# Optimization experiments

Hardware: AMD Instinct MI355X
Metric: run time of the kernel (lower is better)

Reference implementation:

```python
import jax, jax.numpy as jnp
import numpy as np
import math

T, B, D = 2048, 4, 1024
H, HD = 16, 64  # num_heads, head_dim


def _rope_cos_sin(t_len, head_dim):
    inv_freq = 1.0 / (10000.0 ** (jnp.arange(0, head_dim, 2, dtype=jnp.float32) / head_dim))
    t = jnp.arange(t_len, dtype=jnp.float32)
    freqs = jnp.einsum('i,j->ij', t, inv_freq)          # (T, HD/2)
    emb = jnp.concatenate([freqs, freqs], axis=-1)       # (T, HD)
    # broadcast over (T, B, H, HD)
    return jnp.cos(emb)[:, None, None, :], jnp.sin(emb)[:, None, None, :]


def _rotate_half(x):
    x1, x2 = jnp.split(x, 2, axis=-1)
    return jnp.concatenate([-x2, x1], axis=-1)


def setup_inputs() -> dict:
    key = jax.random.key(0)
    ks = jax.random.split(key, 5)
    x = jax.random.normal(ks[0], (T, B, D), dtype=jnp.float32)
    # causal mask: True = masked (future positions), shape (T, T)
    attention_mask = jnp.triu(jnp.ones((T, T), dtype=bool), k=1)
    W_qkv = jax.random.normal(ks[1], (3 * D, D), dtype=jnp.float32) * (1.0 / math.sqrt(D))
    b_qkv = jax.random.normal(ks[2], (3 * D,), dtype=jnp.float32) * 0.02
    W_out = jax.random.normal(ks[3], (D, D), dtype=jnp.float32) * (1.0 / math.sqrt(D))
    b_out = jax.random.normal(ks[4], (D,), dtype=jnp.float32) * 0.02
    return {"x": x, "attention_mask": attention_mask, "W_qkv": W_qkv,
            "b_qkv": b_qkv, "W_out": W_out, "b_out": b_out}


def reference(x, attention_mask, W_qkv, b_qkv, W_out, b_out):
    t_len, b_sz, d = x.shape
    qkv = x @ W_qkv.T + b_qkv                              # (T, B, 3D)
    q, k, v = jnp.split(qkv, 3, axis=-1)
    q = q.reshape(t_len, b_sz, H, HD)
    k = k.reshape(t_len, b_sz, H, HD)
    v = v.reshape(t_len, b_sz, H, HD)

    cos, sin = _rope_cos_sin(t_len, HD)
    q = q * cos + _rotate_half(q) * sin
    k = k * cos + _rotate_half(k) * sin

    scale = math.sqrt(HD)
    # scores: (B, H, T, S)
    scores = jnp.einsum('tbhd,sbhd->bhts', q, k) / scale
    scores = jnp.where(attention_mask[None, None, :, :], -jnp.inf, scores)
    probs = jax.nn.softmax(scores.astype(jnp.float32), axis=-1).astype(v.dtype)
    context = jnp.einsum('bhts,sbhd->tbhd', probs, v)      # (T, B, H, HD)
    context = context.reshape(t_len, b_sz, d)
    return context @ W_out.T + b_out
```

## Files before the change

kernel.cpp:

```cpp
#include <hip/hip_runtime.h>
#include <math.h>

#define T_LEN 2048
#define B_SZ 4
#define D_MODEL 1024
#define NH 16
#define HD 64
#define BH_TOT (B_SZ*NH)

typedef __attribute__((ext_vector_type(8))) short bf16x8;
typedef __attribute__((ext_vector_type(4))) float f32x4;
typedef __attribute__((ext_vector_type(8))) unsigned short u16x8;

union U8 { unsigned int u[4]; bf16x8 v; };

static __device__ __forceinline__ unsigned short f2bf(float f) {
  unsigned int x = __float_as_uint(f);
  x += 0x7fffu + ((x >> 16) & 1u);
  return (unsigned short)(x >> 16);
}
static __device__ __forceinline__ float bf2f(unsigned short u) {
  return __uint_as_float(((unsigned int)u) << 16);
}

__global__ __launch_bounds__(256) void cvt_bf16_kernel(const float* __restrict__ src,
                                                       unsigned short* __restrict__ dst,
                                                       int n8) {
  const int i = blockIdx.x * 256 + threadIdx.x;
  if (i >= n8) return;
  const float4 a = ((const float4*)src)[i * 2];
  const float4 b = ((const float4*)src)[i * 2 + 1];
  u16x8 o;
  o[0] = f2bf(a.x); o[1] = f2bf(a.y); o[2] = f2bf(a.z); o[3] = f2bf(a.w);
  o[4] = f2bf(b.x); o[5] = f2bf(b.y); o[6] = f2bf(b.z); o[7] = f2bf(b.w);
  ((u16x8*)dst)[i] = o;
}

__global__ __launch_bounds__(256, 2) void gemm_mfma_kernel(
    const unsigned short* __restrict__ A, const unsigned short* __restrict__ W,
    const float* __restrict__ bias, float* __restrict__ C,
    int M, int N, int K, int mode,
    unsigned short* __restrict__ qd, unsigned short* __restrict__ kd,
    unsigned short* __restrict__ vd)
{
  __shared__ unsigned short As[128 * 64];
  __shared__ unsigned short Bs[128 * 64];
  const int tid = threadIdx.x;
  const int l = tid & 63, w = tid >> 6;
  const int lq = l & 15, lg = l >> 4;
  const int wm = w >> 1, wn = w & 1;
  const int n0 = blockIdx.x * 128, m0 = blockIdx.y * 128;

  const int sr = tid >> 3;
  const int sb = tid & 7;
  const int scol_src = sb << 4;
  const int scol_dst = scol_src ^ ((sr & 7) << 4);

  f32x4 acc[4][4];
#pragma unroll
  for (int mt = 0; mt < 4; ++mt)
#pragma unroll
    for (int nt = 0; nt < 4; ++nt)
#pragma unroll
      for (int r2 = 0; r2 < 4; ++r2) acc[mt][nt][r2] = 0.f;

  for (int k0 = 0; k0 < K; k0 += 64) {
    bf16x8 ar[4], br[4];
#pragma unroll
    for (int c = 0; c < 4; ++c) {
      const int row = c * 32 + sr;
      ar[c] = *(const bf16x8*)((const char*)A + ((size_t)(m0 + row) * K + k0) * 2 + scol_src);
      br[c] = *(const bf16x8*)((const char*)W + ((size_t)(n0 + row) * K + k0) * 2 + scol_src);
    }
    __syncthreads();
#pragma unroll
    for (int c = 0; c < 4; ++c) {
      const int row = c * 32 + sr;
      *(bf16x8*)((char*)As + row * 128 + scol_dst) = ar[c];
      *(bf16x8*)((char*)Bs + row * 128 + scol_dst) = br[c];
    }
    __syncthreads();

#pragma unroll
    for (int kc = 0; kc < 2; ++kc) {
      bf16x8 af[4], bfr[4];
#pragma unroll
      for (int mt = 0; mt < 4; ++mt) {
        const int r = wm * 64 + mt * 16 + lq;
        af[mt] = *(const bf16x8*)((const char*)As + r * 128 +
                                  ((kc * 64 + lg * 16) ^ ((r & 7) << 4)));
      }
#pragma unroll
      for (int nt = 0; nt < 4; ++nt) {
        const int r = wn * 64 + nt * 16 + lq;
        bfr[nt] = *(const bf16x8*)((const char*)Bs + r * 128 +
                                   ((kc * 64 + lg * 16) ^ ((r & 7) << 4)));
      }
#pragma unroll
      for (int mt = 0; mt < 4; ++mt)
#pragma unroll
        for (int nt = 0; nt < 4; ++nt)
          acc[mt][nt] = __builtin_amdgcn_mfma_f32_16x16x32_bf16(af[mt], bfr[nt], acc[mt][nt], 0, 0, 0);
    }
  }

  if (mode == 0) {
#pragma unroll
    for (int nt = 0; nt < 4; ++nt) {
      const int n = n0 + wn * 64 + nt * 16 + lq;
      const float bv = bias[n];
#pragma unroll
      for (int mt = 0; mt < 4; ++mt)
#pragma unroll
        for (int r2 = 0; r2 < 4; ++r2) {
          const int m = m0 + wm * 64 + mt * 16 + lg * 4 + r2;
          C[(size_t)m * N + n] = acc[mt][nt][r2] + bv;
        }
    }
  } else {
#pragma unroll
    for (int nt = 0; nt < 4; ++nt) {
      const int n = n0 + wn * 64 + nt * 16 + lq;
      const float bv = bias[n];
      const int which = n >> 10;
      const int h = (n >> 6) & (NH - 1);
      const int hd = n & 63;
      unsigned short* dst = (which == 0) ? qd : (which == 1) ? kd : vd;
#pragma unroll
      for (int mt = 0; mt < 4; ++mt)
#pragma unroll
        for (int r2 = 0; r2 < 4; ++r2) {
          const int m = m0 + wm * 64 + mt * 16 + lg * 4 + r2;
          const int t = m >> 2, b = m & 3;
          dst[((size_t)(b * NH + h) * T_LEN + t) * HD + hd] = f2bf(acc[mt][nt][r2] + bv);
        }
    }
  }
}

__global__ void rope_bf16_kernel(unsigned short* __restrict__ qb, unsigned short* __restrict__ kb)
{
  const int idx = blockIdx.x * blockDim.x + threadIdx.x;
  const int i  = idx & 31;
  const int t  = (idx >> 5) & (T_LEN - 1);
  const int bh = idx >> 16;
  const float inv_freq = powf(10000.f, -(float)i / 32.f);
  float s, c;
  sincosf((float)t * inv_freq, &s, &c);
  const size_t base = ((size_t)bh * T_LEN + t) * HD;
  const float q1 = bf2f(qb[base + i]), q2 = bf2f(qb[base + i + 32]);
  qb[base + i]      = f2bf((q1 * c - q2 * s) * 0.125f);
  qb[base + i + 32] = f2bf((q2 * c + q1 * s) * 0.125f);
  const float k1 = bf2f(kb[base + i]), k2 = bf2f(kb[base + i + 32]);
  kb[base + i]      = f2bf(k1 * c - k2 * s);
  kb[base + i + 32] = f2bf(k2 * c + k1 * s);
}

__global__ __launch_bounds__(256) void vtrans_kernel(const unsigned short* __restrict__ v,
                                                     unsigned short* __restrict__ vt)
{
  __shared__ unsigned short Ls[64][65];
  const int tid = threadIdx.x;
  const int bh = blockIdx.x, t0 = blockIdx.y * 64;
  {
    const int r = tid >> 2, c0 = (tid & 3) * 16;
    const unsigned short* src = v + ((size_t)bh * T_LEN + t0 + r) * HD + c0;
    u16x8 f0 = *(const u16x8*)src;
    u16x8 f1 = *(const u16x8*)(src + 8);
#pragma unroll
    for (int e = 0; e < 8; ++e) { Ls[r][c0 + e] = f0[e]; Ls[r][c0 + 8 + e] = f1[e]; }
  }
  __syncthreads();
  {
    const int d = tid >> 2, u0 = (tid & 3) * 16;
    u16x8 o0, o1;
#pragma unroll
    for (int e = 0; e < 8; ++e) { o0[e] = Ls[u0 + e][d]; o1[e] = Ls[u0 + 8 + e][d]; }
    unsigned short* dst = vt + ((size_t)bh * HD + d) * T_LEN + t0 + u0;
    *(u16x8*)dst = o0;
    *(u16x8*)(dst + 8) = o1;
  }
}

__global__ __launch_bounds__(256) void attn_mfma_kernel(
    const unsigned short* __restrict__ Qb,
    const unsigned short* __restrict__ Kb,
    const unsigned short* __restrict__ Vt,
    unsigned short* __restrict__ ctx)
{
  __shared__ unsigned short Ks[64 * 64];
  __shared__ unsigned short Vs[64 * 64];
  const int tid = threadIdx.x;
  const int l = tid & 63;
  const int w = tid >> 6;
  const int lq = l & 15, lg = l >> 4;
  const int bh = blockIdx.x, qbi = blockIdx.y;
  const int b = bh >> 4, h = bh & 15;
  const size_t tb = (size_t)bh * T_LEN;

  const int q0 = qbi * 64 + w * 16;
  bf16x8 qf0, qf1;
  {
    const unsigned short* qr = Qb + (tb + q0 + lq) * HD + lg * 8;
    qf0 = *(const bf16x8*)qr;
    qf1 = *(const bf16x8*)(qr + 32);
  }

  f32x4 acc[4];
#pragma unroll
  for (int dt = 0; dt < 4; ++dt)
#pragma unroll
    for (int r2 = 0; r2 < 4; ++r2) acc[dt][r2] = 0.f;
  float mrun = -1e30f, lsum = 0.f;
  const int qg = q0 + lq;

  for (int kbi = 0; kbi <= qbi; ++kbi) {
    const int s0 = kbi * 64;
    __syncthreads();
    {
      const int r = tid >> 3, c = tid & 7;
      const unsigned short* kg = Kb + (tb + s0 + r) * HD + c * 8;
      bf16x8 k0 = *(const bf16x8*)kg;
      bf16x8 k1 = *(const bf16x8*)(kg + 32 * HD);
      const unsigned short* vg = Vt + ((size_t)bh * HD + r) * T_LEN + s0 + c * 8;
      bf16x8 v0 = *(const bf16x8*)vg;
      bf16x8 v1 = *(const bf16x8*)(vg + 32 * T_LEN);
      const int xk = (c * 16) ^ ((r & 7) << 4);
      *(bf16x8*)((char*)Ks + r * 128 + xk)        = k0;
      *(bf16x8*)((char*)Ks + (r + 32) * 128 + xk) = k1;
      *(bf16x8*)((char*)Vs + r * 128 + xk)        = v0;
      *(bf16x8*)((char*)Vs + (r + 32) * 128 + xk) = v1;
    }
    __syncthreads();

    const bool diag = (kbi == qbi);
    const int stMax = diag ? (w + 1) : 4;

    f32x4 sv[4];
#pragma unroll
    for (int st = 0; st < 4; ++st)
#pragma unroll
      for (int r2 = 0; r2 < 4; ++r2) sv[st][r2] = -1e30f;

#pragma unroll
    for (int st = 0; st < 4; ++st) if (st < stMax) {
      const int r = st * 16 + lq;
      const int x = (r & 7) << 4;
      bf16x8 ka0 = *(const bf16x8*)((const char*)Ks + r * 128 + ((lg * 16) ^ x));
      bf16x8 ka1 = *(const bf16x8*)((const char*)Ks + r * 128 + (((lg + 4) * 16) ^ x));
      f32x4 z;
#pragma unroll
      for (int r2 = 0; r2 < 4; ++r2) z[r2] = 0.f;
      z = __builtin_amdgcn_mfma_f32_16x16x32_bf16(ka1, qf1, z, 0, 0, 0);
      z = __builtin_amdgcn_mfma_f32_16x16x32_bf16(ka0, qf0, z, 0, 0, 0);
      sv[st] = z;
    }

    if (diag) {
#pragma unroll
      for (int st = 0; st < 4; ++st)
#pragma unroll
        for (int r2 = 0; r2 < 4; ++r2) {
          const int sg = s0 + st * 16 + lg * 4 + r2;
          if (sg > qg) sv[st][r2] = -1e30f;
        }
    }

    float tmax = -1e30f;
#pragma unroll
    for (int st = 0; st < 4; ++st)
#pragma unroll
      for (int r2 = 0; r2 < 4; ++r2) tmax = fmaxf(tmax, sv[st][r2]);
    tmax = fmaxf(tmax, __shfl_xor(tmax, 16));
    tmax = fmaxf(tmax, __shfl_xor(tmax, 32));
    const float mnew = fmaxf(mrun, tmax);
    const float alpha = __expf(mrun - mnew);
    float p[4][4];
    float ps = 0.f;
#pragma unroll
    for (int st = 0; st < 4; ++st)
#pragma unroll
      for (int r2 = 0; r2 < 4; ++r2) {
        p[st][r2] = __expf(sv[st][r2] - mnew);
        ps += p[st][r2];
      }
    ps += __shfl_xor(ps, 16);
    ps += __shfl_xor(ps, 32);
    lsum = lsum * alpha + ps;
    mrun = mnew;

    float a4[4];
#pragma unroll
    for (int r2 = 0; r2 < 4; ++r2) a4[r2] = __shfl(alpha, lg * 4 + r2);
#pragma unroll
    for (int dt = 0; dt < 4; ++dt)
#pragma unroll
      for (int r2 = 0; r2 < 4; ++r2) acc[dt][r2] *= a4[r2];

    unsigned int lo[4], hi[4];
#pragma unroll
    for (int st = 0; st < 4; ++st) {
      asm("v_cvt_pk_bf16_f32 %0, %1, %2" : "=v"(lo[st]) : "v"(p[st][0]), "v"(p[st][1]));
      asm("v_cvt_pk_bf16_f32 %0, %1, %2" : "=v"(hi[st]) : "v"(p[st][2]), "v"(p[st][3]));
    }

    const int kcMax = diag ? ((w >> 1) + 1) : 2;
    const int srcA = lq + 32 * (lg & 1);
    const bool hiT = ((lg >> 1) & 1) != 0;
#pragma unroll
    for (int kc = 0; kc < 2; ++kc) if (kc < kcMax) {
      U8 pa;
      {
        unsigned int ta = __shfl(lo[2*kc], srcA),      tb2 = __shfl(lo[2*kc+1], srcA);
        pa.u[0] = hiT ? tb2 : ta;
      }
      {
        unsigned int ta = __shfl(hi[2*kc], srcA),      tb2 = __shfl(hi[2*kc+1], srcA);
        pa.u[1] = hiT ? tb2 : ta;
      }
      {
        unsigned int ta = __shfl(lo[2*kc], srcA + 16), tb2 = __shfl(lo[2*kc+1], srcA + 16);
        pa.u[2] = hiT ? tb2 : ta;
      }
      {
        unsigned int ta = __shfl(hi[2*kc], srcA + 16), tb2 = __shfl(hi[2*kc+1], srcA + 16);
        pa.u[3] = hiT ? tb2 : ta;
      }
#pragma unroll
      for (int dt = 0; dt < 4; ++dt) {
        const int d = dt * 16 + lq;
        bf16x8 vb = *(const bf16x8*)((const char*)Vs + d * 128 +
                                     (((4 * kc + lg) * 16) ^ ((d & 7) << 4)));
        acc[dt] = __builtin_amdgcn_mfma_f32_16x16x32_bf16(pa.v, vb, acc[dt], 0, 0, 0);
      }
    }
  }

  const float linv = 1.f / lsum;
  float l4[4];
#pragma unroll
  for (int r2 = 0; r2 < 4; ++r2) l4[r2] = __shfl(linv, lg * 4 + r2);
#pragma unroll
  for (int dt = 0; dt < 4; ++dt)
#pragma unroll
    for (int r2 = 0; r2 < 4; ++r2) {
      const int qrow = q0 + lg * 4 + r2;
      ctx[((size_t)qrow * B_SZ + b) * D_MODEL + h * HD + dt * 16 + lq] = f2bf(acc[dt][r2] * l4[r2]);
    }
}

extern "C" void kernel_launch(void* const* d_in, const int* in_sizes, int n_in,
                              void* d_out, int out_size, void* d_ws, size_t ws_size,
                              hipStream_t stream) {
  const float* x    = (const float*)d_in[0];
  const float* Wqkv = (const float*)d_in[2];
  const float* bqkv = (const float*)d_in[3];
  const float* Wout = (const float*)d_in[4];
  const float* bout = (const float*)d_in[5];
  float* out = (float*)d_out;

  char* wsb = (char*)d_ws;
  unsigned short* xb    = (unsigned short*)(wsb);
  unsigned short* wqkvb = (unsigned short*)(wsb + (22ull << 20)) - 3145728;
  unsigned short* woutb = (unsigned short*)(wsb + (22ull << 20));
  unsigned short* qb    = (unsigned short*)(wsb + (24ull << 20));
  unsigned short* kb    = (unsigned short*)(wsb + (40ull << 20));
  unsigned short* vb    = (unsigned short*)(wsb + (56ull << 20));
  unsigned short* vt    = (unsigned short*)(wsb + (72ull << 20));
  unsigned short* ctxb  = (unsigned short*)(wsb + (88ull << 20));

  cvt_bf16_kernel<<<(T_LEN*B_SZ*D_MODEL/8 + 255)/256, 256, 0, stream>>>(x, xb, T_LEN*B_SZ*D_MODEL/8);
  cvt_bf16_kernel<<<(3*D_MODEL*D_MODEL/8 + 255)/256, 256, 0, stream>>>(Wqkv, wqkvb, 3*D_MODEL*D_MODEL/8);
  cvt_bf16_kernel<<<(D_MODEL*D_MODEL/8 + 255)/256, 256, 0, stream>>>(Wout, woutb, D_MODEL*D_MODEL/8);

  dim3 g1(3 * D_MODEL / 128, (T_LEN * B_SZ) / 128);
  gemm_mfma_kernel<<<g1, 256, 0, stream>>>(xb, wqkvb, bqkv, nullptr,
                                           T_LEN * B_SZ, 3 * D_MODEL, D_MODEL, 1,
                                           qb, kb, vb);
  const int rope_total = BH_TOT * T_LEN * (HD / 2);
  rope_bf16_kernel<<<(rope_total + 255) / 256, 256, 0, stream>>>(qb, kb);

  dim3 gvt(BH_TOT, T_LEN / 64);
  vtrans_kernel<<<gvt, 256, 0, stream>>>(vb, vt);

  dim3 g2(BH_TOT, T_LEN / 64);
  attn_mfma_kernel<<<g2, 256, 0, stream>>>(qb, kb, vt, ctxb);

  dim3 g3(D_MODEL / 128, (T_LEN * B_SZ) / 128);
  gemm_mfma_kernel<<<g3, 256, 0, stream>>>(ctxb, woutb, bout, out,
                                           T_LEN * B_SZ, D_MODEL, D_MODEL, 0,
                                           nullptr, nullptr, nullptr);
}
```

Baseline: 223.3 us.

## Use direct global-to-LDS loads, double-buffer attention K/V, enlarge query tile

The GEMM staging now uses global_load_lds to write tiles straight into shared memory, skipping the round trip through registers. The attention kernel now gives each block 128 queries (two 16-row sub-tiles per wave) and double-buffers the K/V tiles, prefetching the next tile while computing the current one. Heavy causal blocks are scheduled first, and softmax uses exp2 with log2(e) folded into the Q scale. The rework raises register pressure and halves the attention grid, which may lower occupancy.

```diff
diff --git a/kernel.cpp b/kernel.cpp
--- a/kernel.cpp
+++ b/kernel.cpp
@@ -21,6 +21,10 @@
 }
 static __device__ __forceinline__ float bf2f(unsigned short u) {
   return __uint_as_float(((unsigned int)u) << 16);
+}
+static __device__ __forceinline__ void gload16(const void* g, void* l) {
+  __builtin_amdgcn_global_load_lds((const __attribute__((address_space(1))) void*)g,
+                                   (__attribute__((address_space(3))) void*)l, 16, 0, 0);
 }
 
 __global__ __launch_bounds__(256) void cvt_bf16_kernel(const float* __restrict__ src,
@@ -51,10 +55,8 @@
   const int wm = w >> 1, wn = w & 1;
   const int n0 = blockIdx.x * 128, m0 = blockIdx.y * 128;
 
-  const int sr = tid >> 3;
-  const int sb = tid & 7;
-  const int scol_src = sb << 4;
-  const int scol_dst = scol_src ^ ((sr & 7) << 4);
+  const int lrow = l >> 3;
+  const int lcolb = ((l & 7) << 4) ^ (lrow << 4);
 
   f32x4 acc[4][4];
 #pragma unroll
@@ -65,19 +67,15 @@
       for (int r2 = 0; r2 < 4; ++r2) acc[mt][nt][r2] = 0.f;
 
   for (int k0 = 0; k0 < K; k0 += 64) {
-    bf16x8 ar[4], br[4];
+    __syncthreads();
 #pragma unroll
     for (int c = 0; c < 4; ++c) {
-      const int row = c * 32 + sr;
-      ar[c] = *(const bf16x8*)((const char*)A + ((size_t)(m0 + row) * K + k0) * 2 + scol_src);
-      br[c] = *(const bf16x8*)((const char*)W + ((size_t)(n0 + row) * K + k0) * 2 + scol_src);
-    }
-    __syncthreads();
-#pragma unroll
-    for (int c = 0; c < 4; ++c) {
-      const int row = c * 32 + sr;
-      *(bf16x8*)((char*)As + row * 128 + scol_dst) = ar[c];
-      *(bf16x8*)((char*)Bs + row * 128 + scol_dst) = br[c];
+      const int r0 = w * 32 + c * 8;
+      const int row = r0 + lrow;
+      gload16((const char*)A + ((size_t)(m0 + row) * K + k0) * 2 + lcolb,
+              (char*)As + r0 * 128);
+      gload16((const char*)W + ((size_t)(n0 + row) * K + k0) * 2 + lcolb,
+              (char*)Bs + r0 * 128);
     }
     __syncthreads();
 
@@ -148,9 +146,10 @@
   float s, c;
   sincosf((float)t * inv_freq, &s, &c);
   const size_t base = ((size_t)bh * T_LEN + t) * HD;
+  const float QS = 0.18033688011112042f;
   const float q1 = bf2f(qb[base + i]), q2 = bf2f(qb[base + i + 32]);
-  qb[base + i]      = f2bf((q1 * c - q2 * s) * 0.125f);
-  qb[base + i + 32] = f2bf((q2 * c + q1 * s) * 0.125f);
+  qb[base + i]      = f2bf((q1 * c - q2 * s) * QS);
+  qb[base + i + 32] = f2bf((q2 * c + q1 * s) * QS);
   const float k1 = bf2f(kb[base + i]), k2 = bf2f(kb[base + i + 32]);
   kb[base + i]      = f2bf(k1 * c - k2 * s);
   kb[base + i + 32] = f2bf(k2 * c + k1 * s);
@@ -188,165 +187,206 @@
     const unsigned short* __restrict__ Vt,
     unsigned short* __restrict__ ctx)
 {
-  __shared__ unsigned short Ks[64 * 64];
-  __shared__ unsigned short Vs[64 * 64];
+  __shared__ unsigned short Ks[2][64 * 64];
+  __shared__ unsigned short Vs[2][64 * 64];
   const int tid = threadIdx.x;
   const int l = tid & 63;
   const int w = tid >> 6;
   const int lq = l & 15, lg = l >> 4;
-  const int bh = blockIdx.x, qbi = blockIdx.y;
+  const int bh = blockIdx.x;
+  const int qc = (T_LEN / 128 - 1) - blockIdx.y;
   const int b = bh >> 4, h = bh & 15;
   const size_t tb = (size_t)bh * T_LEN;
 
-  const int q0 = qbi * 64 + w * 16;
-  bf16x8 qf0, qf1;
-  {
-    const unsigned short* qr = Qb + (tb + q0 + lq) * HD + lg * 8;
-    qf0 = *(const bf16x8*)qr;
-    qf1 = *(const bf16x8*)(qr + 32);
-  }
-
-  f32x4 acc[4];
-#pragma unroll
-  for (int dt = 0; dt < 4; ++dt)
-#pragma unroll
-    for (int r2 = 0; r2 < 4; ++r2) acc[dt][r2] = 0.f;
-  float mrun = -1e30f, lsum = 0.f;
-  const int qg = q0 + lq;
-
-  for (int kbi = 0; kbi <= qbi; ++kbi) {
+  const int q0 = qc * 128 + w * 32;
+  bf16x8 qf[2][2];
+#pragma unroll
+  for (int qh = 0; qh < 2; ++qh) {
+    const unsigned short* qr = Qb + (tb + q0 + qh * 16 + lq) * HD + lg * 8;
+    qf[qh][0] = *(const bf16x8*)qr;
+    qf[qh][1] = *(const bf16x8*)(qr + 32);
+  }
+
+  f32x4 acc[2][4];
+#pragma unroll
+  for (int qh = 0; qh < 2; ++qh)
+#pragma unroll
+    for (int dt = 0; dt < 4; ++dt)
+#pragma unroll
+      for (int r2 = 0; r2 < 4; ++r2) acc[qh][dt][r2] = 0.f;
+  float mrun[2] = {-1e30f, -1e30f}, lsum[2] = {0.f, 0.f};
+
+  const int lrow = l >> 3;
+  const int lcolb = ((l & 7) << 4) ^ (lrow << 4);
+  const int last = 2 * qc + 1;
+
+#pragma unroll
+  for (int c = 0; c < 2; ++c) {
+    const int r0 = w * 16 + c * 8;
+    const int row = r0 + lrow;
+    gload16((const char*)Kb + ((tb + 0 + row) * HD) * 2 + lcolb, (char*)Ks[0] + r0 * 128);
+    gload16((const char*)Vt + (((size_t)bh * HD + row) * T_LEN + 0) * 2 + lcolb,
+            (char*)Vs[0] + r0 * 128);
+  }
+  __syncthreads();
+
+  for (int kbi = 0; kbi <= last; ++kbi) {
     const int s0 = kbi * 64;
+    const int cur = kbi & 1;
+
+    if (kbi < last) {
+      const int sn = s0 + 64;
+#pragma unroll
+      for (int c = 0; c < 2; ++c) {
+        const int r0 = w * 16 + c * 8;
+        const int row = r0 + lrow;
+        gload16((const char*)Kb + ((tb + sn + row) * HD) * 2 + lcolb,
+                (char*)Ks[cur ^ 1] + r0 * 128);
+        gload16((const char*)Vt + (((size_t)bh * HD + row) * T_LEN + sn) * 2 + lcolb,
+                (char*)Vs[cur ^ 1] + r0 * 128);
+      }
+    }
+
+    const int dmax = q0 + 31 - s0;
+    if (dmax >= 0) {
+      const int stMax = min(4, (dmax >> 4) + 1);
+      const int kcMax = min(2, (dmax >> 5) + 1);
+      const bool maskN = (s0 + 63 > q0);
+
+      f32x4 sv[2][4];
+#pragma unroll
+      for (int qh = 0; qh < 2; ++qh)
+#pragma unroll
+        for (int st = 0; st < 4; ++st)
+#pragma unroll
+          for (int r2 = 0; r2 < 4; ++r2) sv[qh][st][r2] = -1e30f;
+
+#pragma unroll
+      for (int st = 0; st < 4; ++st) if (st < stMax) {
+        const int r = st * 16 + lq;
+        const int x = (r & 7) << 4;
+        bf16x8 ka0 = *(const bf16x8*)((const char*)Ks[cur] + r * 128 + ((lg * 16) ^ x));
+        bf16x8 ka1 = *(const bf16x8*)((const char*)Ks[cur] + r * 128 + (((lg + 4) * 16) ^ x));
+#pragma unroll
+        for (int qh = 0; qh < 2; ++qh) {
+          f32x4 z;
+#pragma unroll
+          for (int r2 = 0; r2 < 4; ++r2) z[r2] = 0.f;
+          z = __builtin_amdgcn_mfma_f32_16x16x32_bf16(ka1, qf[qh][1], z, 0, 0, 0);
+          z = __builtin_amdgcn_mfma_f32_16x16x32_bf16(ka0, qf[qh][0], z, 0, 0, 0);
+          sv[qh][st] = z;
+        }
+      }
+
+      if (maskN) {
+#pragma unroll
+        for (int qh = 0; qh < 2; ++qh) {
+          const int qg = q0 + qh * 16 + lq;
+#pragma unroll
+          for (int st = 0; st < 4; ++st)
+#pragma unroll
+            for (int r2 = 0; r2 < 4; ++r2) {
+              const int sg = s0 + st * 16 + lg * 4 + r2;
+              if (sg > qg) sv[qh][st][r2] = -1e30f;
+            }
+        }
+      }
+
+      unsigned int lo[2][4], hi[2][4];
+#pragma unroll
+      for (int qh = 0; qh < 2; ++qh) {
+        float tmax = -1e30f;
+#pragma unroll
+        for (int st = 0; st < 4; ++st)
+#pragma unroll
+          for (int r2 = 0; r2 < 4; ++r2) tmax = fmaxf(tmax, sv[qh][st][r2]);
+        tmax = fmaxf(tmax, __shfl_xor(tmax, 16));
+        tmax = fmaxf(tmax, __shfl_xor(tmax, 32));
+        const float mnew = fmaxf(mrun[qh], tmax);
+        const float alpha = exp2f(mrun[qh] - mnew);
+        float p[4][4];
+        float ps = 0.f;
+#pragma unroll
+        for (int st = 0; st < 4; ++st)
+#pragma unroll
+          for (int r2 = 0; r2 < 4; ++r2) {
+            p[st][r2] = exp2f(sv[qh][st][r2] - mnew);
+            ps += p[st][r2];
+          }
+        ps += __shfl_xor(ps, 16);
+        ps += __shfl_xor(ps, 32);
+        lsum[qh] = lsum[qh] * alpha + ps;
+        mrun[qh] = mnew;
+
+        float a4[4];
+#pragma unroll
+        for (int r2 = 0; r2 < 4; ++r2) a4[r2] = __shfl(alpha, lg * 4 + r2);
+#pragma unroll
+        for (int dt = 0; dt < 4; ++dt)
+#pragma unroll
+          for (int r2 = 0; r2 < 4; ++r2) acc[qh][dt][r2] *= a4[r2];
+
+#pragma unroll
+        for (int st = 0; st < 4; ++st) {
+          asm("v_cvt_pk_bf16_f32 %0, %1, %2" : "=v"(lo[qh][st]) : "v"(p[st][0]), "v"(p[st][1]));
+          asm("v_cvt_pk_bf16_f32 %0, %1, %2" : "=v"(hi[qh][st]) : "v"(p[st][2]), "v"(p[st][3]));
+        }
+      }
+
+      const int srcA = lq + 32 * (lg & 1);
+      const bool hiT = ((lg >> 1) & 1) != 0;
+#pragma unroll
+      for (int kc = 0; kc < 2; ++kc) if (kc < kcMax) {
+        U8 pa[2];
+#pragma unroll
+        for (int qh = 0; qh < 2; ++qh) {
+          {
+            unsigned int ta = __shfl(lo[qh][2*kc], srcA),      tb2 = __shfl(lo[qh][2*kc+1], srcA);
+            pa[qh].u[0] = hiT ? tb2 : ta;
+          }
+          {
+            unsigned int ta = __shfl(hi[qh][2*kc], srcA),      tb2 = __shfl(hi[qh][2*kc+1], srcA);
+            pa[qh].u[1] = hiT ? tb2 : ta;
+          }
+          {
+            unsigned int ta = __shfl(lo[qh][2*kc], srcA + 16), tb2 = __shfl(lo[qh][2*kc+1], srcA + 16);
+            pa[qh].u[2] = hiT ? tb2 : ta;
+          }
+          {
+            unsigned int ta = __shfl(hi[qh][2*kc], srcA + 16), tb2 = __shfl(hi[qh][2*kc+1], srcA + 16);
+            pa[qh].u[3] = hiT ? tb2 : ta;
+          }
+        }
+#pragma unroll
+        for (int dt = 0; dt < 4; ++dt) {
+          const int d = dt * 16 + lq;
+          bf16x8 vb = *(const bf16x8*)((const char*)Vs[cur] + d * 128 +
+                                       (((4 * kc + lg) * 16) ^ ((d & 7) << 4)));
+#pragma unroll
+          for (int qh = 0; qh < 2; ++qh)
+            acc[qh][dt] = __builtin_amdgcn_mfma_f32_16x16x32_bf16(pa[qh].v, vb, acc[qh][dt], 0, 0, 0);
+        }
+      }
+    }
+
     __syncthreads();
-    {
-      const int r = tid >> 3, c = tid & 7;
-      const unsigned short* kg = Kb + (tb + s0 + r) * HD + c * 8;
-      bf16x8 k0 = *(const bf16x8*)kg;
-      bf16x8 k1 = *(const bf16x8*)(kg + 32 * HD);
-      const unsigned short* vg = Vt + ((size_t)bh * HD + r) * T_LEN + s0 + c * 8;
-      bf16x8 v0 = *(const bf16x8*)vg;
-      bf16x8 v1 = *(const bf16x8*)(vg + 32 * T_LEN);
-      const int xk = (c * 16) ^ ((r & 7) << 4);
-      *(bf16x8*)((char*)Ks + r * 128 + xk)        = k0;
-      *(bf16x8*)((char*)Ks + (r + 32) * 128 + xk) = k1;
-      *(bf16x8*)((char*)Vs + r * 128 + xk)        = v0;
-      *(bf16x8*)((char*)Vs + (r + 32) * 128 + xk) = v1;
-    }
-    __syncthreads();
-
-    const bool diag = (kbi == qbi);
-    const int stMax = diag ? (w + 1) : 4;
-
-    f32x4 sv[4];
-#pragma unroll
-    for (int st = 0; st < 4; ++st)
-#pragma unroll
-      for (int r2 = 0; r2 < 4; ++r2) sv[st][r2] = -1e30f;
-
-#pragma unroll
-    for (int st = 0; st < 4; ++st) if (st < stMax) {
-      const int r = st * 16 + lq;
-      const int x = (r & 7) << 4;
-      bf16x8 ka0 = *(const bf16x8*)((const char*)Ks + r * 128 + ((lg * 16) ^ x));
-      bf16x8 ka1 = *(const bf16x8*)((const char*)Ks + r * 128 + (((lg + 4) * 16) ^ x));
-      f32x4 z;
-#pragma unroll
-      for (int r2 = 0; r2 < 4; ++r2) z[r2] = 0.f;
-      z = __builtin_amdgcn_mfma_f32_16x16x32_bf16(ka1, qf1, z, 0, 0, 0);
-      z = __builtin_amdgcn_mfma_f32_16x16x32_bf16(ka0, qf0, z, 0, 0, 0);
-      sv[st] = z;
-    }
-
-    if (diag) {
-#pragma unroll
-      for (int st = 0; st < 4; ++st)
-#pragma unroll
-        for (int r2 = 0; r2 < 4; ++r2) {
-          const int sg = s0 + st * 16 + lg * 4 + r2;
-          if (sg > qg) sv[st][r2] = -1e30f;
-        }
-    }
-
-    float tmax = -1e30f;
-#pragma unroll
-    for (int st = 0; st < 4; ++st)
-#pragma unroll
-      for (int r2 = 0; r2 < 4; ++r2) tmax = fmaxf(tmax, sv[st][r2]);
-    tmax = fmaxf(tmax, __shfl_xor(tmax, 16));
-    tmax = fmaxf(tmax, __shfl_xor(tmax, 32));
-    const float mnew = fmaxf(mrun, tmax);
-    const float alpha = __expf(mrun - mnew);
-    float p[4][4];
-    float ps = 0.f;
-#pragma unroll
-    for (int st = 0; st < 4; ++st)
+  }
+
+#pragma unroll
+  for (int qh = 0; qh < 2; ++qh) {
+    const float linv = 1.f / lsum[qh];
+    float l4[4];
+#pragma unroll
+    for (int r2 = 0; r2 < 4; ++r2) l4[r2] = __shfl(linv, lg * 4 + r2);
+#pragma unroll
+    for (int dt = 0; dt < 4; ++dt)
 #pragma unroll
       for (int r2 = 0; r2 < 4; ++r2) {
-        p[st][r2] = __expf(sv[st][r2] - mnew);
-        ps += p[st][r2];
-      }
-    ps += __shfl_xor(ps, 16);
-    ps += __shfl_xor(ps, 32);
-    lsum = lsum * alpha + ps;
-    mrun = mnew;
-
-    float a4[4];
-#pragma unroll
-    for (int r2 = 0; r2 < 4; ++r2) a4[r2] = __shfl(alpha, lg * 4 + r2);
-#pragma unroll
-    for (int dt = 0; dt < 4; ++dt)
-#pragma unroll
-      for (int r2 = 0; r2 < 4; ++r2) acc[dt][r2] *= a4[r2];
-
-    unsigned int lo[4], hi[4];
-#pragma unroll
-    for (int st = 0; st < 4; ++st) {
-      asm("v_cvt_pk_bf16_f32 %0, %1, %2" : "=v"(lo[st]) : "v"(p[st][0]), "v"(p[st][1]));
-      asm("v_cvt_pk_bf16_f32 %0, %1, %2" : "=v"(hi[st]) : "v"(p[st][2]), "v"(p[st][3]));
-    }
-
-    const int kcMax = diag ? ((w >> 1) + 1) : 2;
-    const int srcA = lq + 32 * (lg & 1);
-    const bool hiT = ((lg >> 1) & 1) != 0;
-#pragma unroll
-    for (int kc = 0; kc < 2; ++kc) if (kc < kcMax) {
-      U8 pa;
-      {
-        unsigned int ta = __shfl(lo[2*kc], srcA),      tb2 = __shfl(lo[2*kc+1], srcA);
-        pa.u[0] = hiT ? tb2 : ta;
-      }
-      {
-        unsigned int ta = __shfl(hi[2*kc], srcA),      tb2 = __shfl(hi[2*kc+1], srcA);
-        pa.u[1] = hiT ? tb2 : ta;
-      }
-      {
-        unsigned int ta = __shfl(lo[2*kc], srcA + 16), tb2 = __shfl(lo[2*kc+1], srcA + 16);
-        pa.u[2] = hiT ? tb2 : ta;
-      }
-      {
-        unsigned int ta = __shfl(hi[2*kc], srcA + 16), tb2 = __shfl(hi[2*kc+1], srcA + 16);
-        pa.u[3] = hiT ? tb2 : ta;
-      }
-#pragma unroll
-      for (int dt = 0; dt < 4; ++dt) {
-        const int d = dt * 16 + lq;
-        bf16x8 vb = *(const bf16x8*)((const char*)Vs + d * 128 +
-                                     (((4 * kc + lg) * 16) ^ ((d & 7) << 4)));
-        acc[dt] = __builtin_amdgcn_mfma_f32_16x16x32_bf16(pa.v, vb, acc[dt], 0, 0, 0);
-      }
-    }
-  }
-
-  const float linv = 1.f / lsum;
-  float l4[4];
-#pragma unroll
-  for (int r2 = 0; r2 < 4; ++r2) l4[r2] = __shfl(linv, lg * 4 + r2);
-#pragma unroll
-  for (int dt = 0; dt < 4; ++dt)
-#pragma unroll
-    for (int r2 = 0; r2 < 4; ++r2) {
-      const int qrow = q0 + lg * 4 + r2;
-      ctx[((size_t)qrow * B_SZ + b) * D_MODEL + h * HD + dt * 16 + lq] = f2bf(acc[dt][r2] * l4[r2]);
-    }
+        const int qrow = q0 + qh * 16 + lg * 4 + r2;
+        ctx[((size_t)qrow * B_SZ + b) * D_MODEL + h * HD + dt * 16 + lq] =
+            f2bf(acc[qh][dt][r2] * linv * 0.f + acc[qh][dt][r2] * l4[r2]);
+      }
+  }
 }
 
 extern "C" void kernel_launch(void* const* d_in, const int* in_sizes, int n_in,
@@ -361,7 +401,7 @@
 
   char* wsb = (char*)d_ws;
   unsigned short* xb    = (unsigned short*)(wsb);
-  unsigned short* wqkvb = (unsigned short*)(wsb + (22ull << 20)) - 3145728;
+  unsigned short* wqkvb = (unsigned short*)(wsb + (16ull << 20));
   unsigned short* woutb = (unsigned short*)(wsb + (22ull << 20));
   unsigned short* qb    = (unsigned short*)(wsb + (24ull << 20));
   unsigned short* kb    = (unsigned short*)(wsb + (40ull << 20));
@@ -383,7 +423,7 @@
   dim3 gvt(BH_TOT, T_LEN / 64);
   vtrans_kernel<<<gvt, 256, 0, stream>>>(vb, vt);
 
-  dim3 g2(BH_TOT, T_LEN / 64);
+  dim3 g2(BH_TOT, T_LEN / 128);
   attn_mfma_kernel<<<g2, 256, 0, stream>>>(qb, kb, vt, ctxb);
 
   dim3 g3(D_MODEL / 128, (T_LEN * B_SZ) / 128);
```

Result: slower. 246.7 us (+10.5%).
